# Kernel optimization log

Measured on AMD Instinct MI355X. Metric: run time of the kernel, lower is better.

## Reference

```python
import jax, jax.numpy as jnp
import numpy as np

BN_EPS = 1e-5

def _bn_eval(x, gamma, beta):
    # Fresh torch BatchNorm1d in eval mode: running_mean=0, running_var=1
    return x * (gamma / jnp.sqrt(1.0 + BN_EPS)) + beta

def setup_inputs() -> dict:
    key = jax.random.key(0)
    ks = jax.random.split(key, 10)
    Q, K, H, W, D = 64, 128, 24, 8, 128
    L = H * W            # seq_len = 192
    FF = 2048            # dim_feedforward
    q_feat = jax.random.normal(ks[0], (Q, H, W, D), dtype=jnp.float32)
    g_feat = jax.random.normal(ks[1], (K, H, W, D), dtype=jnp.float32)
    se = jax.random.normal(ks[2], (L, L), dtype=jnp.float32)
    score_embed = (se + se.T).reshape(1, 1, L, L)
    s = 1.0 / np.sqrt(D)
    fc0_w = jax.random.uniform(ks[3], (D, D), jnp.float32, -s, s)
    fc0_b = jax.random.uniform(ks[4], (D,), jnp.float32, -s, s)
    s2 = 1.0 / np.sqrt(L)
    fc2_w = jax.random.uniform(ks[5], (FF, L), jnp.float32, -s2, s2)
    fc2_b = jax.random.uniform(ks[6], (FF,), jnp.float32, -s2, s2)
    s3 = 1.0 / np.sqrt(FF)
    fc3_w = jax.random.uniform(ks[7], (1, FF), jnp.float32, -s3, s3)
    fc3_b = jax.random.uniform(ks[8], (1,), jnp.float32, -s3, s3)
    bn1_g = jnp.ones((1,)); bn1_b = jnp.zeros((1,))
    bn2_g = jnp.ones((FF,)) + 0.1 * jax.random.normal(ks[9], (FF,), jnp.float32)
    bn2_b = jnp.zeros((FF,))
    bn3_g = jnp.ones((1,)); bn3_b = jnp.zeros((1,))
    return dict(q_feat=q_feat, g_feat=g_feat, score_embed=score_embed,
                fc0_w=fc0_w, fc0_b=fc0_b, fc2_w=fc2_w, fc2_b=fc2_b,
                fc3_w=fc3_w, fc3_b=fc3_b, bn1_g=bn1_g, bn1_b=bn1_b,
                bn2_g=bn2_g, bn2_b=bn2_b, bn3_g=bn3_g, bn3_b=bn3_b)

def reference(q_feat, g_feat, score_embed, fc0_w, fc0_b, fc2_w, fc2_b,
              fc3_w, fc3_b, bn1_g, bn1_b, bn2_g, bn2_b, bn3_g, bn3_b):
    Q = q_feat.shape[0]
    K = g_feat.shape[0]
    D = q_feat.shape[-1]
    L = score_embed.shape[-1]  # seq_len
    tgt = q_feat.reshape(Q, L, D)
    mem = g_feat.reshape(K, L, D)
    query = tgt @ fc0_w.T + fc0_b      # [Q, L, D]
    key_ = mem @ fc0_w.T + fc0_b       # [K, L, D]
    # [Q, K, L(s), L(t)] score, modulated by broadcast sigmoid bias
    score = jnp.einsum('qtd,ksd->qkst', query, key_) * jax.nn.sigmoid(score_embed)
    score = score.reshape(Q * K, L, L)
    # max over s and over t, concatenated per pair -> [QK, 2L]
    score = jnp.concatenate([score.max(axis=1), score.max(axis=2)], axis=-1)
    score = score.reshape(-1, L)       # [2*QK, L]
    score = _bn_eval(score, bn1_g, bn1_b)
    score = score @ fc2_w.T + fc2_b    # [2*QK, FF]
    score = _bn_eval(score, bn2_g, bn2_b)
    score = jax.nn.relu(score)
    score = score @ fc3_w.T + fc3_b    # [2*QK, 1]
    score = score.reshape(-1, 2).sum(axis=-1, keepdims=True)  # [QK, 1]
    score = _bn_eval(score, bn3_g, bn3_b)
    return score.reshape(Q, K)
```

## Files before the change

### kernel.cpp

```cpp
#include <hip/hip_runtime.h>

#define LL 192
#define FF 2048

typedef __attribute__((__ext_vector_type__(8)))  __bf16 bf16x8;
typedef __attribute__((__ext_vector_type__(4)))  __bf16 bf16x4;
typedef __attribute__((__ext_vector_type__(4)))  float  f32x4;

#define MFMA16(a, b, c) __builtin_amdgcn_mfma_f32_16x16x32_bf16((a), (b), (c), 0, 0, 0)


__launch_bounds__(256, 2)
__global__ void proj_prep_kernel(const float* __restrict__ qf_in,
                                 const float* __restrict__ gf_in,
                                 const float* __restrict__ fc0w,
                                 const float* __restrict__ fc0b,
                                 const float* __restrict__ se,
                                 const float* __restrict__ fc2w,
                                 const float* __restrict__ fc2b,
                                 const float* __restrict__ bn2g,
                                 const float* __restrict__ bn2b,
                                 const float* __restrict__ fc3w,
                                 __bf16* __restrict__ kfragA,
                                 __bf16* __restrict__ qfrag16,
                                 __bf16* __restrict__ sig16,
                                 __bf16* __restrict__ fc2w_bf,
                                 float* __restrict__ h2,
                                 float* __restrict__ bb2,
                                 float* __restrict__ f3)
{
    int bx = blockIdx.x, tid = threadIdx.x;
    if (bx >= 1152) {
        int i0 = (bx - 1152) * 256 + tid;
        const int stride = 160 * 256;
        const float c1 = rsqrtf(1.f + 1e-5f);
        for (int i = i0; i < LL * LL; i += stride) {
            int r = i & 3, lane = (i >> 2) & 63, tile = i >> 8;
            int jt = tile % 12, st = tile / 12;
            int s = st * 16 + (lane >> 4) * 4 + r;
            int t = jt * 16 + (lane & 15);
            sig16[i] = (__bf16)(1.f / (1.f + __expf(-se[s * 192 + t])));
        }
        for (int i = i0; i < FF * LL; i += stride)
            fc2w_bf[i] = (__bf16)fc2w[i];
        for (int i = i0; i < FF; i += stride) {
            float h = bn2g[i] * c1;
            h2[i]  = h;
            bb2[i] = fc2b[i] * h + bn2b[i];
            f3[i]  = fc3w[i];
        }
        return;
    }
    __shared__ __bf16 Xs[32][136];
    __shared__ __bf16 Ws[128][136];
    __shared__ __bf16 Os[4096];
    const float* src = (bx < 384) ? (qf_in + (size_t)bx * (32 * 128))
                                  : (gf_in + (size_t)(bx - 384) * (32 * 128));
#pragma unroll
    for (int it = 0; it < 4; ++it) {
        int e = (it * 256 + tid) * 4;
        int r = e >> 7, c = e & 127;
        float4 v = *reinterpret_cast<const float4*>(src + e);
        bf16x4 xv;
        xv[0] = (__bf16)v.x; xv[1] = (__bf16)v.y;
        xv[2] = (__bf16)v.z; xv[3] = (__bf16)v.w;
        *reinterpret_cast<bf16x4*>(&Xs[r][c]) = xv;
    }
#pragma unroll
    for (int it = 0; it < 16; ++it) {
        int e = (it * 256 + tid) * 4;
        int r = e >> 7, c = e & 127;
        float4 v = *reinterpret_cast<const float4*>(fc0w + e);
        bf16x4 xv;
        xv[0] = (__bf16)v.x; xv[1] = (__bf16)v.y;
        xv[2] = (__bf16)v.z; xv[3] = (__bf16)v.w;
        *reinterpret_cast<bf16x4*>(&Ws[r][c]) = xv;
    }
    __syncthreads();

    int wv = tid >> 6, lane = tid & 63, quad = lane >> 4, l16 = lane & 15;
    int n0 = wv * 32;
    f32x4 acc[2][2];
#pragma unroll
    for (int m = 0; m < 2; ++m)
#pragma unroll
        for (int n = 0; n < 2; ++n) acc[m][n] = (f32x4){0.f, 0.f, 0.f, 0.f};
#pragma unroll
    for (int ks = 0; ks < 4; ++ks) {
        bf16x8 a0 = *reinterpret_cast<const bf16x8*>(&Xs[l16][ks * 32 + quad * 8]);
        bf16x8 a1 = *reinterpret_cast<const bf16x8*>(&Xs[16 + l16][ks * 32 + quad * 8]);
        bf16x8 b0 = *reinterpret_cast<const bf16x8*>(&Ws[n0 + l16][ks * 32 + quad * 8]);
        bf16x8 b1 = *reinterpret_cast<const bf16x8*>(&Ws[n0 + 16 + l16][ks * 32 + quad * 8]);
        acc[0][0] = MFMA16(a0, b0, acc[0][0]);
        acc[0][1] = MFMA16(a0, b1, acc[0][1]);
        acc[1][0] = MFMA16(a1, b0, acc[1][0]);
        acc[1][1] = MFMA16(a1, b1, acc[1][1]);
    }
#pragma unroll
    for (int mt = 0; mt < 2; ++mt)
#pragma unroll
        for (int nt = 0; nt < 2; ++nt) {
            int d = n0 + nt * 16 + l16;
            float bv = fc0b[d];
            int abase = mt * 2048 + (d >> 5) * 512 + ((d >> 3) & 3) * 128 + (d & 7);
#pragma unroll
            for (int r = 0; r < 4; ++r)
                Os[abase + (quad * 4 + r) * 8] = (__bf16)(acc[mt][nt][r] + bv);
        }
    __syncthreads();

    int row0 = bx * 32;
    __bf16* dst;
    if (bx < 384) {
        int qi = row0 / 192, tg0 = (row0 % 192) >> 4;
        dst = qfrag16 + qi * 24576 + tg0 * 2048;
    } else {
        int rk0 = row0 - 12288;
        int ki = rk0 / 192, sg0 = (rk0 % 192) >> 4;
        dst = kfragA + ki * 24576 + sg0 * 2048;
    }
#pragma unroll
    for (int it = 0; it < 2; ++it) {
        int e = (it * 256 + tid) * 8;
        *reinterpret_cast<bf16x8*>(dst + e) =
            *reinterpret_cast<const bf16x8*>(&Os[e]);
    }
}

__launch_bounds__(384, 2)
__global__ void score_kernel(const __bf16* __restrict__ kfragA,
                             const __bf16* __restrict__ qfrag16,
                             const __bf16* __restrict__ sig16,
                             const float* __restrict__ bn1g,
                             const float* __restrict__ bn1b,
                             __bf16* __restrict__ Sred)
{
    __shared__ __bf16 qf[24576];
    __shared__ __bf16 rowT[32][200];
    __shared__ __bf16 colmax[192][6];

    int tid = threadIdx.x;
    int q = blockIdx.x & 63;
    int kbase = (blockIdx.x >> 6) << 3;
    int w = tid >> 6, lane = tid & 63, quad = lane >> 4, l16 = lane & 15;

    const __bf16* qsrc = qfrag16 + (size_t)q * 24576;
#pragma unroll
    for (int it = 0; it < 8; ++it) {
        int e = (it * 384 + tid) * 8;
        *reinterpret_cast<bf16x8*>(&qf[e]) =
            *reinterpret_cast<const bf16x8*>(qsrc + e);
    }
    const float g1c = bn1g[0] * rsqrtf(1.f + 1e-5f);
    const float b1v = bn1b[0];

    bf16x4 sgv[2][12];
#pragma unroll
    for (int i = 0; i < 2; ++i)
#pragma unroll
        for (int jt = 0; jt < 12; ++jt)
            sgv[i][jt] = *reinterpret_cast<const bf16x4*>(
                sig16 + ((size_t)((2 * w + i) * 12 + jt) * 64 + lane) * 4);
    __syncthreads();

    for (int kk = 0; kk < 8; ++kk) {
        int kidx = kbase + kk;
        const __bf16* kp = kfragA + (size_t)kidx * 24576 + lane * 8;
#pragma unroll
        for (int jg = 0; jg < 2; ++jg) {
            f32x4 acc[2][6];
#pragma unroll
            for (int i = 0; i < 2; ++i)
#pragma unroll
                for (int j = 0; j < 6; ++j) acc[i][j] = (f32x4){0.f, 0.f, 0.f, 0.f};

#pragma unroll
            for (int ks = 0; ks < 4; ++ks) {
                bf16x8 a0 = *reinterpret_cast<const bf16x8*>(
                    kp + ((2 * w + 0) * 4 + ks) * 512);
                bf16x8 a1 = *reinterpret_cast<const bf16x8*>(
                    kp + ((2 * w + 1) * 4 + ks) * 512);
#pragma unroll
                for (int j = 0; j < 6; ++j) {
                    bf16x8 b = *reinterpret_cast<const bf16x8*>(
                        &qf[((jg * 6 + j) * 4 + ks) * 512 + lane * 8]);
                    acc[0][j] = MFMA16(a0, b, acc[0][j]);
                    acc[1][j] = MFMA16(a1, b, acc[1][j]);
                }
            }

            float cm[6];
#pragma unroll
            for (int j = 0; j < 6; ++j) cm[j] = -3.0e38f;
#pragma unroll
            for (int i = 0; i < 2; ++i) {
                float rm0 = -3.0e38f, rm1 = -3.0e38f, rm2 = -3.0e38f, rm3 = -3.0e38f;
#pragma unroll
                for (int j = 0; j < 6; ++j) {
                    bf16x4 sv = sgv[i][jg * 6 + j];
                    float v0 = acc[i][j][0] * (float)sv[0];
                    float v1 = acc[i][j][1] * (float)sv[1];
                    float v2 = acc[i][j][2] * (float)sv[2];
                    float v3 = acc[i][j][3] * (float)sv[3];
                    rm0 = fmaxf(rm0, v0); rm1 = fmaxf(rm1, v1);
                    rm2 = fmaxf(rm2, v2); rm3 = fmaxf(rm3, v3);
                    cm[j] = fmaxf(cm[j], fmaxf(fmaxf(v0, v1), fmaxf(v2, v3)));
                }
                bf16x4 pk;
                pk[0] = (__bf16)rm0; pk[1] = (__bf16)rm1;
                pk[2] = (__bf16)rm2; pk[3] = (__bf16)rm3;
                *reinterpret_cast<bf16x4*>(
                    &rowT[jg * 16 + l16][32 * w + 16 * i + quad * 4]) = pk;
            }
#pragma unroll
            for (int j = 0; j < 6; ++j) {
                cm[j] = fmaxf(cm[j], __shfl_xor(cm[j], 16, 64));
                cm[j] = fmaxf(cm[j], __shfl_xor(cm[j], 32, 64));
            }
            if (quad == 0) {
#pragma unroll
                for (int j = 0; j < 6; ++j)
                    colmax[(jg * 6 + j) * 16 + l16][w] = (__bf16)cm[j];
            }
        }
        __syncthreads();

        if (tid < 192) {
            size_t pb = (size_t)(q * 128 + kidx) * 384;
            float m0 = (float)colmax[tid][0];
#pragma unroll
            for (int u = 1; u < 6; ++u) m0 = fmaxf(m0, (float)colmax[tid][u]);
            Sred[pb + tid] = (__bf16)(m0 * g1c + b1v);
            float m1 = -3.0e38f;
#pragma unroll
            for (int c = 0; c < 32; ++c)
                m1 = fmaxf(m1, (float)rowT[c][tid]);
            Sred[pb + 192 + tid] = (__bf16)(m1 * g1c + b1v);
        }
        __syncthreads();
    }
}

__launch_bounds__(512, 1)
__global__ void mlp_kernel(const __bf16* __restrict__ Sred,
                           const __bf16* __restrict__ fc2w_bf,
                           const float* __restrict__ h2,
                           const float* __restrict__ bb2,
                           const float* __restrict__ f3,
                           const float* __restrict__ fc3b,
                           const float* __restrict__ bn3g,
                           const float* __restrict__ bn3b,
                           float* __restrict__ out)
{
    __shared__ __bf16 As[64][200];
    __shared__ float  psum_lds[8][64];
    int bx = blockIdx.x, tid = threadIdx.x;
    const __bf16* asrc = Sred + (size_t)bx * (64 * 192);
#pragma unroll
    for (int it = 0; it < 3; ++it) {
        int e = (it * 512 + tid) * 8;
        int r = e / 192, c = e - r * 192;
        *reinterpret_cast<bf16x8*>(&As[r][c]) =
            *reinterpret_cast<const bf16x8*>(asrc + e);
    }
    __syncthreads();

    int wv = tid >> 6, lane = tid & 63, quad = lane >> 4, l16 = lane & 15;
    bf16x8 af[4][6];
#pragma unroll
    for (int m = 0; m < 4; ++m)
#pragma unroll
        for (int kk = 0; kk < 6; ++kk)
            af[m][kk] = *reinterpret_cast<const bf16x8*>(
                &As[m * 16 + l16][kk * 32 + quad * 8]);

    float ps[4][4] = {{0.f,0.f,0.f,0.f},{0.f,0.f,0.f,0.f},
                      {0.f,0.f,0.f,0.f},{0.f,0.f,0.f,0.f}};
    for (int nt = 0; nt < 16; ++nt) {
        int n0 = wv * 256 + nt * 16;
        f32x4 acc[4];
#pragma unroll
        for (int m = 0; m < 4; ++m) acc[m] = (f32x4){0.f, 0.f, 0.f, 0.f};
        const __bf16* bp = fc2w_bf + (size_t)(n0 + l16) * 192 + quad * 8;
#pragma unroll
        for (int kk = 0; kk < 6; ++kk) {
            bf16x8 b = *reinterpret_cast<const bf16x8*>(bp + kk * 32);
#pragma unroll
            for (int m = 0; m < 4; ++m) acc[m] = MFMA16(af[m][kk], b, acc[m]);
        }
        int n = n0 + l16;
        float hh = h2[n], bb = bb2[n], ffv = f3[n];
#pragma unroll
        for (int m = 0; m < 4; ++m)
#pragma unroll
            for (int r = 0; r < 4; ++r)
                ps[m][r] += fmaxf(acc[m][r] * hh + bb, 0.f) * ffv;
    }
#pragma unroll
    for (int m = 0; m < 4; ++m)
#pragma unroll
        for (int r = 0; r < 4; ++r) {
            float v = ps[m][r];
            v += __shfl_xor(v, 1, 64);
            v += __shfl_xor(v, 2, 64);
            v += __shfl_xor(v, 4, 64);
            v += __shfl_xor(v, 8, 64);
            if (l16 == 0) psum_lds[wv][m * 16 + quad * 4 + r] = v;
        }
    __syncthreads();
    if (tid < 32) {
        float s = 0.f;
#pragma unroll
        for (int w = 0; w < 8; ++w)
            s += psum_lds[w][2 * tid] + psum_lds[w][2 * tid + 1];
        const float c1 = rsqrtf(1.f + 1e-5f);
        out[bx * 32 + tid] = (s + 2.f * fc3b[0]) * (bn3g[0] * c1) + bn3b[0];
    }
}

extern "C" void kernel_launch(void* const* d_in, const int* in_sizes, int n_in,
                              void* d_out, int out_size, void* d_ws, size_t ws_size,
                              hipStream_t stream)
{
    const float* q_feat = (const float*)d_in[0];
    const float* g_feat = (const float*)d_in[1];
    const float* se     = (const float*)d_in[2];
    const float* fc0w   = (const float*)d_in[3];
    const float* fc0b   = (const float*)d_in[4];
    const float* fc2w   = (const float*)d_in[5];
    const float* fc2b   = (const float*)d_in[6];
    const float* fc3w   = (const float*)d_in[7];
    const float* fc3b   = (const float*)d_in[8];
    const float* bn1g   = (const float*)d_in[9];
    const float* bn1b   = (const float*)d_in[10];
    const float* bn2g   = (const float*)d_in[11];
    const float* bn2b   = (const float*)d_in[12];
    const float* bn3g   = (const float*)d_in[13];
    const float* bn3b   = (const float*)d_in[14];
    float* out = (float*)d_out;

    char* ws = (char*)d_ws;
    __bf16* kfragA   = (__bf16*)(ws);
    __bf16* qfrag16  = (__bf16*)(ws +  6291456);
    __bf16* sig16    = (__bf16*)(ws +  9437184);
    __bf16* fc2w_bf  = (__bf16*)(ws +  9543680);
    float*  h2       = (float*) (ws + 10330112);
    float*  bb2      = (float*) (ws + 10338304);
    float*  f3       = (float*) (ws + 10346496);
    __bf16* Sred     = (__bf16*)(ws + 10354688);

    proj_prep_kernel<<<1312, 256, 0, stream>>>(q_feat, g_feat, fc0w, fc0b, se,
                                               fc2w, fc2b, bn2g, bn2b, fc3w,
                                               kfragA, qfrag16, sig16, fc2w_bf,
                                               h2, bb2, f3);
    score_kernel<<<1024, 384, 0, stream>>>(kfragA, qfrag16, sig16, bn1g, bn1b, Sred);
    mlp_kernel<<<256, 512, 0, stream>>>(Sred, fc2w_bf, h2, bb2, f3,
                                        fc3b, bn3g, bn3b, out);
}
```

Baseline: 241.9 us.

## Give each wave whole (q,k) pairs in score kernel, drop LDS and barriers

The score kernel now assigns two full (q,k) pairs to each wave, with 4 waves per block, instead of splitting one pair's rows across 6 waves. This removes the shared-memory staging of the q fragments, the rowT/colmax exchange buffers and both block barriers. Row and column maxima are reduced in registers with cross-lane shuffles and written straight to Sred. The q fragments and sigmoid weights are now read from global memory or cache on every tile rather than from LDS, which raises global and L2 traffic.

```diff
diff --git a/kernel.cpp b/kernel.cpp
--- a/kernel.cpp
+++ b/kernel.cpp
@@ -127,7 +127,7 @@
     }
 }
 
-__launch_bounds__(384, 2)
+__launch_bounds__(256, 2)
 __global__ void score_kernel(const __bf16* __restrict__ kfragA,
                              const __bf16* __restrict__ qfrag16,
                              const __bf16* __restrict__ sig16,
@@ -135,109 +135,117 @@
                              const float* __restrict__ bn1b,
                              __bf16* __restrict__ Sred)
 {
-    __shared__ __bf16 qf[24576];
-    __shared__ __bf16 rowT[32][200];
-    __shared__ __bf16 colmax[192][6];
-
     int tid = threadIdx.x;
     int q = blockIdx.x & 63;
     int kbase = (blockIdx.x >> 6) << 3;
     int w = tid >> 6, lane = tid & 63, quad = lane >> 4, l16 = lane & 15;
-
-    const __bf16* qsrc = qfrag16 + (size_t)q * 24576;
-#pragma unroll
-    for (int it = 0; it < 8; ++it) {
-        int e = (it * 384 + tid) * 8;
-        *reinterpret_cast<bf16x8*>(&qf[e]) =
-            *reinterpret_cast<const bf16x8*>(qsrc + e);
-    }
     const float g1c = bn1g[0] * rsqrtf(1.f + 1e-5f);
     const float b1v = bn1b[0];
-
-    bf16x4 sgv[2][12];
-#pragma unroll
-    for (int i = 0; i < 2; ++i)
-#pragma unroll
-        for (int jt = 0; jt < 12; ++jt)
-            sgv[i][jt] = *reinterpret_cast<const bf16x4*>(
-                sig16 + ((size_t)((2 * w + i) * 12 + jt) * 64 + lane) * 4);
-    __syncthreads();
-
-    for (int kk = 0; kk < 8; ++kk) {
-        int kidx = kbase + kk;
+    const __bf16* qbase = qfrag16 + (size_t)q * 24576 + lane * 8;
+
+    for (int pp = 0; pp < 2; ++pp) {
+        int kidx = kbase + 2 * w + pp;
         const __bf16* kp = kfragA + (size_t)kidx * 24576 + lane * 8;
-#pragma unroll
-        for (int jg = 0; jg < 2; ++jg) {
-            f32x4 acc[2][6];
-#pragma unroll
-            for (int i = 0; i < 2; ++i)
-#pragma unroll
-                for (int j = 0; j < 6; ++j) acc[i][j] = (f32x4){0.f, 0.f, 0.f, 0.f};
-
-#pragma unroll
-            for (int ks = 0; ks < 4; ++ks) {
-                bf16x8 a0 = *reinterpret_cast<const bf16x8*>(
-                    kp + ((2 * w + 0) * 4 + ks) * 512);
-                bf16x8 a1 = *reinterpret_cast<const bf16x8*>(
-                    kp + ((2 * w + 1) * 4 + ks) * 512);
-#pragma unroll
-                for (int j = 0; j < 6; ++j) {
-                    bf16x8 b = *reinterpret_cast<const bf16x8*>(
-                        &qf[((jg * 6 + j) * 4 + ks) * 512 + lane * 8]);
-                    acc[0][j] = MFMA16(a0, b, acc[0][j]);
-                    acc[1][j] = MFMA16(a1, b, acc[1][j]);
+        size_t ob = (size_t)(q * 128 + kidx) * 384;
+
+        float cmv[12];
+#pragma unroll
+        for (int jt = 0; jt < 12; ++jt) cmv[jt] = -3.0e38f;
+
+        for (int sg = 0; sg < 4; ++sg) {
+            float rm[3][4];
+#pragma unroll
+            for (int i = 0; i < 3; ++i)
+#pragma unroll
+                for (int r = 0; r < 4; ++r) rm[i][r] = -3.0e38f;
+
+#pragma unroll
+            for (int qt = 0; qt < 4; ++qt) {
+                bf16x4 sgv[3][3];
+#pragma unroll
+                for (int i = 0; i < 3; ++i)
+#pragma unroll
+                    for (int j = 0; j < 3; ++j)
+                        sgv[i][j] = *reinterpret_cast<const bf16x4*>(
+                            sig16 + ((size_t)((3 * sg + i) * 12 + qt * 3 + j) * 64
+                                     + lane) * 4);
+
+                f32x4 acc[3][3];
+#pragma unroll
+                for (int i = 0; i < 3; ++i)
+#pragma unroll
+                    for (int j = 0; j < 3; ++j)
+                        acc[i][j] = (f32x4){0.f, 0.f, 0.f, 0.f};
+
+#pragma unroll
+                for (int ks = 0; ks < 4; ++ks) {
+                    bf16x8 a[3];
+#pragma unroll
+                    for (int i = 0; i < 3; ++i)
+                        a[i] = *reinterpret_cast<const bf16x8*>(
+                            kp + ((3 * sg + i) * 4 + ks) * 512);
+#pragma unroll
+                    for (int j = 0; j < 3; ++j) {
+                        bf16x8 b = *reinterpret_cast<const bf16x8*>(
+                            qbase + ((qt * 3 + j) * 4 + ks) * 512);
+#pragma unroll
+                        for (int i = 0; i < 3; ++i)
+                            acc[i][j] = MFMA16(a[i], b, acc[i][j]);
+                    }
+                }
+
+#pragma unroll
+                for (int j = 0; j < 3; ++j) {
+                    float cj = -3.0e38f;
+#pragma unroll
+                    for (int i = 0; i < 3; ++i) {
+                        float v0 = acc[i][j][0] * (float)sgv[i][j][0];
+                        float v1 = acc[i][j][1] * (float)sgv[i][j][1];
+                        float v2 = acc[i][j][2] * (float)sgv[i][j][2];
+                        float v3 = acc[i][j][3] * (float)sgv[i][j][3];
+                        rm[i][0] = fmaxf(rm[i][0], v0);
+                        rm[i][1] = fmaxf(rm[i][1], v1);
+                        rm[i][2] = fmaxf(rm[i][2], v2);
+                        rm[i][3] = fmaxf(rm[i][3], v3);
+                        cj = fmaxf(cj, fmaxf(fmaxf(v0, v1), fmaxf(v2, v3)));
+                    }
+                    cmv[qt * 3 + j] = fmaxf(cmv[qt * 3 + j], cj);
                 }
             }
 
-            float cm[6];
-#pragma unroll
-            for (int j = 0; j < 6; ++j) cm[j] = -3.0e38f;
-#pragma unroll
-            for (int i = 0; i < 2; ++i) {
-                float rm0 = -3.0e38f, rm1 = -3.0e38f, rm2 = -3.0e38f, rm3 = -3.0e38f;
-#pragma unroll
-                for (int j = 0; j < 6; ++j) {
-                    bf16x4 sv = sgv[i][jg * 6 + j];
-                    float v0 = acc[i][j][0] * (float)sv[0];
-                    float v1 = acc[i][j][1] * (float)sv[1];
-                    float v2 = acc[i][j][2] * (float)sv[2];
-                    float v3 = acc[i][j][3] * (float)sv[3];
-                    rm0 = fmaxf(rm0, v0); rm1 = fmaxf(rm1, v1);
-                    rm2 = fmaxf(rm2, v2); rm3 = fmaxf(rm3, v3);
-                    cm[j] = fmaxf(cm[j], fmaxf(fmaxf(v0, v1), fmaxf(v2, v3)));
+#pragma unroll
+            for (int i = 0; i < 3; ++i)
+#pragma unroll
+                for (int r = 0; r < 4; ++r) {
+                    float v = rm[i][r];
+                    v = fmaxf(v, __shfl_xor(v, 1, 64));
+                    v = fmaxf(v, __shfl_xor(v, 2, 64));
+                    v = fmaxf(v, __shfl_xor(v, 4, 64));
+                    v = fmaxf(v, __shfl_xor(v, 8, 64));
+                    rm[i][r] = v;
                 }
-                bf16x4 pk;
-                pk[0] = (__bf16)rm0; pk[1] = (__bf16)rm1;
-                pk[2] = (__bf16)rm2; pk[3] = (__bf16)rm3;
-                *reinterpret_cast<bf16x4*>(
-                    &rowT[jg * 16 + l16][32 * w + 16 * i + quad * 4]) = pk;
+            if (l16 == 0) {
+#pragma unroll
+                for (int i = 0; i < 3; ++i) {
+                    bf16x4 pk;
+                    pk[0] = (__bf16)(rm[i][0] * g1c + b1v);
+                    pk[1] = (__bf16)(rm[i][1] * g1c + b1v);
+                    pk[2] = (__bf16)(rm[i][2] * g1c + b1v);
+                    pk[3] = (__bf16)(rm[i][3] * g1c + b1v);
+                    *reinterpret_cast<bf16x4*>(
+                        &Sred[ob + 192 + 48 * sg + 16 * i + quad * 4]) = pk;
+                }
             }
-#pragma unroll
-            for (int j = 0; j < 6; ++j) {
-                cm[j] = fmaxf(cm[j], __shfl_xor(cm[j], 16, 64));
-                cm[j] = fmaxf(cm[j], __shfl_xor(cm[j], 32, 64));
-            }
-            if (quad == 0) {
-#pragma unroll
-                for (int j = 0; j < 6; ++j)
-                    colmax[(jg * 6 + j) * 16 + l16][w] = (__bf16)cm[j];
-            }
-        }
-        __syncthreads();
-
-        if (tid < 192) {
-            size_t pb = (size_t)(q * 128 + kidx) * 384;
-            float m0 = (float)colmax[tid][0];
-#pragma unroll
-            for (int u = 1; u < 6; ++u) m0 = fmaxf(m0, (float)colmax[tid][u]);
-            Sred[pb + tid] = (__bf16)(m0 * g1c + b1v);
-            float m1 = -3.0e38f;
-#pragma unroll
-            for (int c = 0; c < 32; ++c)
-                m1 = fmaxf(m1, (float)rowT[c][tid]);
-            Sred[pb + 192 + tid] = (__bf16)(m1 * g1c + b1v);
-        }
-        __syncthreads();
+        }
+
+#pragma unroll
+        for (int jt = 0; jt < 12; ++jt) {
+            float v = cmv[jt];
+            v = fmaxf(v, __shfl_xor(v, 16, 64));
+            v = fmaxf(v, __shfl_xor(v, 32, 64));
+            if (lane < 16)
+                Sred[ob + jt * 16 + lane] = (__bf16)(v * g1c + b1v);
+        }
     }
 }
 
@@ -353,7 +361,7 @@
                                                fc2w, fc2b, bn2g, bn2b, fc3w,
                                                kfragA, qfrag16, sig16, fc2w_bf,
                                                h2, bb2, f3);
-    score_kernel<<<1024, 384, 0, stream>>>(kfragA, qfrag16, sig16, bn1g, bn1b, Sred);
+    score_kernel<<<1024, 256, 0, stream>>>(kfragA, qfrag16, sig16, bn1g, bn1b, Sred);
     mlp_kernel<<<256, 512, 0, stream>>>(Sred, fc2w_bf, h2, bb2, f3,
                                         fc3b, bn3g, bn3b, out);
 }
```

Measured after the change: 536.9 us. +121.9%, slower.

## Keep query fragments in registers and stage key tiles in LDS for score kernel

Applied to the files above, without the earlier changes.

The score kernel is restructured to 4 waves per block instead of 6. Each wave now holds its 48 query columns as MFMA B-fragments in registers for the whole block. Each key's 192x128 tile is copied into shared memory per iteration instead of being read directly from global memory. The column max over s is reduced entirely within a wave with shuffles and written straight out. The row max is pre-reduced with lane shuffles, so the shared transpose buffer shrinks from 32 to 16 partials. In exchange, the per-iteration global-to-LDS copy is not overlapped with compute, sigmoid weights are reloaded from global inside the loop, and fewer threads run per block.

```diff
diff --git a/kernel.cpp b/kernel.cpp
--- a/kernel.cpp
+++ b/kernel.cpp
@@ -127,7 +127,7 @@
     }
 }
 
-__launch_bounds__(384, 2)
+__launch_bounds__(256, 2)
 __global__ void score_kernel(const __bf16* __restrict__ kfragA,
                              const __bf16* __restrict__ qfrag16,
                              const __bf16* __restrict__ sig16,
@@ -135,109 +135,124 @@
                              const float* __restrict__ bn1b,
                              __bf16* __restrict__ Sred)
 {
-    __shared__ __bf16 qf[24576];
-    __shared__ __bf16 rowT[32][200];
-    __shared__ __bf16 colmax[192][6];
+    __shared__ __bf16 Abuf[24576];
+    __shared__ __bf16 rowT4[16][200];
 
     int tid = threadIdx.x;
     int q = blockIdx.x & 63;
     int kbase = (blockIdx.x >> 6) << 3;
     int w = tid >> 6, lane = tid & 63, quad = lane >> 4, l16 = lane & 15;
-
-    const __bf16* qsrc = qfrag16 + (size_t)q * 24576;
-#pragma unroll
-    for (int it = 0; it < 8; ++it) {
-        int e = (it * 384 + tid) * 8;
-        *reinterpret_cast<bf16x8*>(&qf[e]) =
-            *reinterpret_cast<const bf16x8*>(qsrc + e);
-    }
     const float g1c = bn1g[0] * rsqrtf(1.f + 1e-5f);
     const float b1v = bn1b[0];
 
-    bf16x4 sgv[2][12];
-#pragma unroll
-    for (int i = 0; i < 2; ++i)
-#pragma unroll
-        for (int jt = 0; jt < 12; ++jt)
-            sgv[i][jt] = *reinterpret_cast<const bf16x4*>(
-                sig16 + ((size_t)((2 * w + i) * 12 + jt) * 64 + lane) * 4);
-    __syncthreads();
-
+    bf16x8 Bf[3][4];
+    {
+        const __bf16* qb = qfrag16 + (size_t)q * 24576 + lane * 8;
+#pragma unroll
+        for (int j = 0; j < 3; ++j)
+#pragma unroll
+            for (int ks = 0; ks < 4; ++ks)
+                Bf[j][ks] = *reinterpret_cast<const bf16x8*>(
+                    qb + ((3 * w + j) * 4 + ks) * 512);
+    }
+
+#pragma unroll 1
     for (int kk = 0; kk < 8; ++kk) {
         int kidx = kbase + kk;
-        const __bf16* kp = kfragA + (size_t)kidx * 24576 + lane * 8;
-#pragma unroll
-        for (int jg = 0; jg < 2; ++jg) {
-            f32x4 acc[2][6];
+        const __bf16* kp = kfragA + (size_t)kidx * 24576;
+#pragma unroll
+        for (int it = 0; it < 12; ++it) {
+            int e = (it * 256 + tid) * 8;
+            *reinterpret_cast<bf16x8*>(&Abuf[e]) =
+                *reinterpret_cast<const bf16x8*>(kp + e);
+        }
+        __syncthreads();
+
+        size_t ob = (size_t)(q * 128 + kidx) * 384;
+        float cm0 = -3.0e38f, cm1 = -3.0e38f, cm2 = -3.0e38f;
+
+#pragma unroll 1
+        for (int sc = 0; sc < 6; ++sc) {
+            f32x4 acc[2][3];
 #pragma unroll
             for (int i = 0; i < 2; ++i)
 #pragma unroll
-                for (int j = 0; j < 6; ++j) acc[i][j] = (f32x4){0.f, 0.f, 0.f, 0.f};
+                for (int j = 0; j < 3; ++j)
+                    acc[i][j] = (f32x4){0.f, 0.f, 0.f, 0.f};
 
 #pragma unroll
             for (int ks = 0; ks < 4; ++ks) {
                 bf16x8 a0 = *reinterpret_cast<const bf16x8*>(
-                    kp + ((2 * w + 0) * 4 + ks) * 512);
+                    &Abuf[((sc * 2 + 0) * 4 + ks) * 512 + lane * 8]);
                 bf16x8 a1 = *reinterpret_cast<const bf16x8*>(
-                    kp + ((2 * w + 1) * 4 + ks) * 512);
-#pragma unroll
-                for (int j = 0; j < 6; ++j) {
-                    bf16x8 b = *reinterpret_cast<const bf16x8*>(
-                        &qf[((jg * 6 + j) * 4 + ks) * 512 + lane * 8]);
-                    acc[0][j] = MFMA16(a0, b, acc[0][j]);
-                    acc[1][j] = MFMA16(a1, b, acc[1][j]);
+                    &Abuf[((sc * 2 + 1) * 4 + ks) * 512 + lane * 8]);
+#pragma unroll
+                for (int j = 0; j < 3; ++j) {
+                    acc[0][j] = MFMA16(a0, Bf[j][ks], acc[0][j]);
+                    acc[1][j] = MFMA16(a1, Bf[j][ks], acc[1][j]);
                 }
             }
 
-            float cm[6];
-#pragma unroll
-            for (int j = 0; j < 6; ++j) cm[j] = -3.0e38f;
 #pragma unroll
             for (int i = 0; i < 2; ++i) {
                 float rm0 = -3.0e38f, rm1 = -3.0e38f, rm2 = -3.0e38f, rm3 = -3.0e38f;
 #pragma unroll
-                for (int j = 0; j < 6; ++j) {
-                    bf16x4 sv = sgv[i][jg * 6 + j];
+                for (int j = 0; j < 3; ++j) {
+                    bf16x4 sv = *reinterpret_cast<const bf16x4*>(
+                        sig16 + ((size_t)((sc * 2 + i) * 12 + 3 * w + j) * 64
+                                 + lane) * 4);
                     float v0 = acc[i][j][0] * (float)sv[0];
                     float v1 = acc[i][j][1] * (float)sv[1];
                     float v2 = acc[i][j][2] * (float)sv[2];
                     float v3 = acc[i][j][3] * (float)sv[3];
                     rm0 = fmaxf(rm0, v0); rm1 = fmaxf(rm1, v1);
                     rm2 = fmaxf(rm2, v2); rm3 = fmaxf(rm3, v3);
-                    cm[j] = fmaxf(cm[j], fmaxf(fmaxf(v0, v1), fmaxf(v2, v3)));
+                    float cj = fmaxf(fmaxf(v0, v1), fmaxf(v2, v3));
+                    if (j == 0) cm0 = fmaxf(cm0, cj);
+                    else if (j == 1) cm1 = fmaxf(cm1, cj);
+                    else cm2 = fmaxf(cm2, cj);
                 }
-                bf16x4 pk;
-                pk[0] = (__bf16)rm0; pk[1] = (__bf16)rm1;
-                pk[2] = (__bf16)rm2; pk[3] = (__bf16)rm3;
-                *reinterpret_cast<bf16x4*>(
-                    &rowT[jg * 16 + l16][32 * w + 16 * i + quad * 4]) = pk;
+                rm0 = fmaxf(rm0, __shfl_xor(rm0, 1, 64));
+                rm0 = fmaxf(rm0, __shfl_xor(rm0, 2, 64));
+                rm1 = fmaxf(rm1, __shfl_xor(rm1, 1, 64));
+                rm1 = fmaxf(rm1, __shfl_xor(rm1, 2, 64));
+                rm2 = fmaxf(rm2, __shfl_xor(rm2, 1, 64));
+                rm2 = fmaxf(rm2, __shfl_xor(rm2, 2, 64));
+                rm3 = fmaxf(rm3, __shfl_xor(rm3, 1, 64));
+                rm3 = fmaxf(rm3, __shfl_xor(rm3, 2, 64));
+                if ((l16 & 3) == 0) {
+                    bf16x4 pk;
+                    pk[0] = (__bf16)rm0; pk[1] = (__bf16)rm1;
+                    pk[2] = (__bf16)rm2; pk[3] = (__bf16)rm3;
+                    *reinterpret_cast<bf16x4*>(
+                        &rowT4[(l16 >> 2) * 4 + w][sc * 32 + 16 * i + quad * 4]) = pk;
+                }
             }
-#pragma unroll
-            for (int j = 0; j < 6; ++j) {
-                cm[j] = fmaxf(cm[j], __shfl_xor(cm[j], 16, 64));
-                cm[j] = fmaxf(cm[j], __shfl_xor(cm[j], 32, 64));
+        }
+
+        {
+            float v0 = cm0, v1 = cm1, v2 = cm2;
+            v0 = fmaxf(v0, __shfl_xor(v0, 16, 64));
+            v0 = fmaxf(v0, __shfl_xor(v0, 32, 64));
+            v1 = fmaxf(v1, __shfl_xor(v1, 16, 64));
+            v1 = fmaxf(v1, __shfl_xor(v1, 32, 64));
+            v2 = fmaxf(v2, __shfl_xor(v2, 16, 64));
+            v2 = fmaxf(v2, __shfl_xor(v2, 32, 64));
+            if (quad == 0) {
+                Sred[ob + (3 * w + 0) * 16 + l16] = (__bf16)(v0 * g1c + b1v);
+                Sred[ob + (3 * w + 1) * 16 + l16] = (__bf16)(v1 * g1c + b1v);
+                Sred[ob + (3 * w + 2) * 16 + l16] = (__bf16)(v2 * g1c + b1v);
             }
-            if (quad == 0) {
-#pragma unroll
-                for (int j = 0; j < 6; ++j)
-                    colmax[(jg * 6 + j) * 16 + l16][w] = (__bf16)cm[j];
-            }
         }
         __syncthreads();
 
         if (tid < 192) {
-            size_t pb = (size_t)(q * 128 + kidx) * 384;
-            float m0 = (float)colmax[tid][0];
-#pragma unroll
-            for (int u = 1; u < 6; ++u) m0 = fmaxf(m0, (float)colmax[tid][u]);
-            Sred[pb + tid] = (__bf16)(m0 * g1c + b1v);
             float m1 = -3.0e38f;
 #pragma unroll
-            for (int c = 0; c < 32; ++c)
-                m1 = fmaxf(m1, (float)rowT[c][tid]);
-            Sred[pb + 192 + tid] = (__bf16)(m1 * g1c + b1v);
-        }
-        __syncthreads();
+            for (int c = 0; c < 16; ++c)
+                m1 = fmaxf(m1, (float)rowT4[c][tid]);
+            Sred[ob + 192 + tid] = (__bf16)(m1 * g1c + b1v);
+        }
     }
 }
 
@@ -353,7 +368,7 @@
                                                fc2w, fc2b, bn2g, bn2b, fc3w,
                                                kfragA, qfrag16, sig16, fc2w_bf,
                                                h2, bb2, f3);
-    score_kernel<<<1024, 384, 0, stream>>>(kfragA, qfrag16, sig16, bn1g, bn1b, Sred);
+    score_kernel<<<1024, 256, 0, stream>>>(kfragA, qfrag16, sig16, bn1g, bn1b, Sred);
     mlp_kernel<<<256, 512, 0, stream>>>(Sred, fc2w_bf, h2, bb2, f3,
                                         fc3b, bn3g, bn3b, out);
 }
```

After: 249.9 us. 3.3% more time.
